# Performance work log

Measured on AMD Instinct MI355X. Metric: run time of the kernel, lower is better.

Reference implementation:

```python
import jax, jax.numpy as jnp
import numpy as np

B, N, D, H = 4, 2048, 512, 8
HD = D // H


def setup_inputs() -> dict:
    key = jax.random.key(0)
    ks = jax.random.split(key, 10)
    x = jax.random.normal(ks[0], (B, N, D), dtype=jnp.float32)
    adj = (jax.random.uniform(ks[1], (N, N)) < 0.1).astype(jnp.float32)
    s = 1.0 / np.sqrt(D)
    Wq = jax.random.normal(ks[2], (D, D), dtype=jnp.float32) * s
    Wk = jax.random.normal(ks[3], (D, D), dtype=jnp.float32) * s
    Wv = jax.random.normal(ks[4], (D, D), dtype=jnp.float32) * s
    Wo = jax.random.normal(ks[5], (D, D), dtype=jnp.float32) * s
    bq = jnp.zeros((D,), jnp.float32)
    bk = jnp.zeros((D,), jnp.float32)
    bv = jnp.zeros((D,), jnp.float32)
    bo = jnp.zeros((D,), jnp.float32)
    return {"x": x, "adj": adj, "Wq": Wq, "bq": bq, "Wk": Wk, "bk": bk,
            "Wv": Wv, "bv": bv, "Wo": Wo, "bo": bo}


def reference(x, adj, Wq, bq, Wk, bk, Wv, bv, Wo, bo):
    b, n, d = x.shape
    q = (x @ Wq + bq).reshape(b, n, H, HD)
    k = (x @ Wk + bk).reshape(b, n, H, HD)
    v = (x @ Wv + bv).reshape(b, n, H, HD)
    scores = jnp.einsum('bqhd,bkhd->bhqk', q, k) / jnp.sqrt(jnp.float32(HD))
    scores = scores + (1.0 - adj)[None, None, :, :] * (-1e9)
    attn = jax.nn.softmax(scores, axis=-1)
    out = jnp.einsum('bhqk,bkhd->bqhd', attn, v).reshape(b, n, d)
    return out @ Wo + bo
```

## Files before the change

### kernel.cpp

```cpp
#include <hip/hip_runtime.h>
#include <math.h>

#define NB    4
#define NSEQ  2048
#define DMODEL 512
#define NH    8
#define HDIM  64
#define STR   72
#define LOG2E 1.44269504088896f

typedef __attribute__((ext_vector_type(8))) short short8;
typedef __attribute__((ext_vector_type(4))) float f32x4;
typedef __attribute__((ext_vector_type(16))) float f32x16;
#define MFMA16 __builtin_amdgcn_mfma_f32_16x16x32_bf16
#define MFMA32 __builtin_amdgcn_mfma_f32_32x32x16_bf16
#define EXP2F __builtin_amdgcn_exp2f

__device__ __forceinline__ unsigned short f2bf(float f) {
    union { float f; unsigned int u; } v; v.f = f;
    unsigned int u = v.u;
    unsigned int r = (u + 0x7FFFu + ((u >> 16) & 1u)) >> 16;
    return (unsigned short)r;
}
__device__ __forceinline__ short8 andmask8(short8 p, unsigned bits) {
    union { short8 s; uint4 u; } x; x.s = p;
    x.u.x &= ((bits &   1u) ? 0xFFFFu : 0u) | ((bits &   2u) ? 0xFFFF0000u : 0u);
    x.u.y &= ((bits &   4u) ? 0xFFFFu : 0u) | ((bits &   8u) ? 0xFFFF0000u : 0u);
    x.u.z &= ((bits &  16u) ? 0xFFFFu : 0u) | ((bits &  32u) ? 0xFFFF0000u : 0u);
    x.u.w &= ((bits &  64u) ? 0xFFFFu : 0u) | ((bits & 128u) ? 0xFFFF0000u : 0u);
    return x.s;
}
__device__ __forceinline__ void async16(void* lds, const void* g) {
    __builtin_amdgcn_global_load_lds(
        (const __attribute__((address_space(1))) unsigned int*)g,
        (__attribute__((address_space(3))) unsigned int*)lds, 16, 0, 0);
}

__global__ __launch_bounds__(256) void mask_kernel(const float* __restrict__ adj,
                                                   unsigned long long* __restrict__ Mb) {
    const int w    = blockIdx.x * 4 + (threadIdx.x >> 6);
    const int lane = threadIdx.x & 63;
    const int q  = w >> 5;
    const int kt = w & 31;
    float a = adj[(size_t)q * NSEQ + kt * 64 + lane];
    unsigned long long m = __ballot(a > 0.5f);
    if (lane == 0) Mb[(size_t)kt * NSEQ + q] = m;
}

__global__ __launch_bounds__(256) void split_x_kernel(const float* __restrict__ x,
                                                      unsigned short* __restrict__ xhi) {
    int gid = blockIdx.x * 256 + threadIdx.x;
    float4 a = ((const float4*)x)[gid];
    ushort4 h4;
    h4.x = f2bf(a.x); h4.y = f2bf(a.y); h4.z = f2bf(a.z); h4.w = f2bf(a.w);
    ((ushort4*)xhi)[gid] = h4;
}

__global__ __launch_bounds__(256) void split_wt_kernel(
    const float* __restrict__ Wq, const float* __restrict__ Wk,
    const float* __restrict__ Wv, const float* __restrict__ Wo,
    unsigned short* __restrict__ Wthi)
{
    __shared__ float tile[32][33];
    const int m = blockIdx.z;
    const float* W = (m == 0) ? Wq : (m == 1) ? Wk : (m == 2) ? Wv : Wo;
    const int k0 = blockIdx.x * 32, n0 = blockIdx.y * 32;
    const int tx = threadIdx.x & 31, ty = threadIdx.x >> 5;
    #pragma unroll
    for (int i = 0; i < 4; ++i)
        tile[ty * 4 + i][tx] = W[(size_t)(k0 + ty * 4 + i) * DMODEL + n0 + tx];
    __syncthreads();
    const size_t base = ((size_t)m * DMODEL) * DMODEL;
    #pragma unroll
    for (int i = 0; i < 4; ++i) {
        float f = tile[tx][ty * 4 + i];
        size_t idx = base + (size_t)(n0 + ty * 4 + i) * DMODEL + k0 + tx;
        Wthi[idx] = f2bf(f);
    }
}

__device__ __forceinline__ void gemm_k_loop(
    const unsigned short* __restrict__ Ah,
    const unsigned short* __restrict__ Bh,
    char* smem, f32x4 acc[4][4])
{
    const int t    = threadIdx.x;
    const int lane = t & 63;
    const int wid  = t >> 6;
    const int quad = lane >> 4, l16 = lane & 15;
    const int wm   = wid >> 1,  wn  = wid & 1;

    unsigned short* As_h = (unsigned short*)(smem);
    unsigned short* Bs_h = (unsigned short*)(smem + 8192);

    const int ci0 = t, ci1 = 256 + t;
    const int r0 = ci0 >> 2, r1 = ci1 >> 2;
    const int c0 = (ci0 & 3) ^ ((r0 >> 1) & 3);
    const int c1 = (ci1 & 3) ^ ((r1 >> 1) & 3);
    const char* gAh = (const char*)Ah;
    const char* gBh = (const char*)Bh;
    const int ca = quad ^ ((l16 >> 1) & 3);

    for (int k0 = 0; k0 < DMODEL; k0 += 32) {
        const int kb = k0 * 2;
        async16(As_h + ci0 * 8, gAh + r0 * 1024 + kb + c0 * 16);
        async16(As_h + ci1 * 8, gAh + r1 * 1024 + kb + c1 * 16);
        async16(Bs_h + ci0 * 8, gBh + r0 * 1024 + kb + c0 * 16);
        async16(Bs_h + ci1 * 8, gBh + r1 * 1024 + kb + c1 * 16);
        __syncthreads();

        short8 ah[4], bh[4];
        #pragma unroll
        for (int i = 0; i < 4; ++i) {
            const int Ra = wm * 64 + i * 16 + l16;
            ah[i] = *(const short8*)(As_h + Ra * 32 + ca * 8);
            const int Rb = wn * 64 + i * 16 + l16;
            bh[i] = *(const short8*)(Bs_h + Rb * 32 + ca * 8);
        }
        #pragma unroll
        for (int mi = 0; mi < 4; ++mi)
            #pragma unroll
            for (int ni = 0; ni < 4; ++ni)
                acc[mi][ni] = MFMA16(ah[mi], bh[ni], acc[mi][ni], 0, 0, 0);
        __syncthreads();
    }
}

__global__ __launch_bounds__(256, 2) void qkv_mfma_kernel(
    const unsigned short* __restrict__ xhi,
    const unsigned short* __restrict__ Wthi,
    const float* __restrict__ bq, const float* __restrict__ bk, const float* __restrict__ bv,
    unsigned short* __restrict__ Qhi,
    unsigned short* __restrict__ Khi,
    unsigned short* __restrict__ Vt)
{
    __shared__ __align__(16) char smem[33280];
    const int t    = threadIdx.x;
    const int lane = t & 63;
    const int wid  = t >> 6;
    const int quad = lane >> 4, l16 = lane & 15;
    const int wm   = wid >> 1,  wn  = wid & 1;

    const int row0 = blockIdx.x * 128;
    const int yb   = blockIdx.y;
    const int mtx  = yb >> 2;
    const int col0 = (yb & 3) * 128;

    f32x4 acc[4][4];
    #pragma unroll
    for (int i = 0; i < 4; ++i)
        #pragma unroll
        for (int j = 0; j < 4; ++j) acc[i][j] = (f32x4){0.f, 0.f, 0.f, 0.f};

    const size_t wslot = (size_t)mtx * DMODEL * DMODEL;
    gemm_k_loop(xhi + (size_t)row0 * DMODEL,
                Wthi + wslot + (size_t)col0 * DMODEL, smem, acc);

    const float* bias = (mtx == 0) ? bq : (mtx == 1) ? bk : bv;
    float bcol[4];
    #pragma unroll
    for (int ni = 0; ni < 4; ++ni) bcol[ni] = bias[col0 + wn * 64 + ni * 16 + l16];
    const int h = (col0 + wn * 64) >> 6;

    if (mtx < 2) {
        const float scale = (mtx == 0) ? (0.125f * LOG2E) : 1.0f;
        unsigned short* hig = (mtx == 0) ? Qhi : Khi;
        #pragma unroll
        for (int mi = 0; mi < 4; ++mi) {
            #pragma unroll
            for (int reg = 0; reg < 4; ++reg) {
                const int r = row0 + wm * 64 + mi * 16 + quad * 4 + reg;
                const int b = r >> 11, n = r & 2047;
                const size_t rowbase = ((size_t)(b * NH + h) * NSEQ + n) * HDIM;
                #pragma unroll
                for (int ni = 0; ni < 4; ++ni)
                    hig[rowbase + ni * 16 + l16] =
                        f2bf((acc[mi][ni][reg] + bcol[ni]) * scale);
            }
        }
    } else {
        unsigned short* vt = (unsigned short*)smem + (size_t)wid * 64 * 65;
        #pragma unroll
        for (int mi = 0; mi < 4; ++mi)
            #pragma unroll
            for (int ni = 0; ni < 4; ++ni)
                #pragma unroll
                for (int reg = 0; reg < 4; ++reg)
                    vt[(mi * 16 + quad * 4 + reg) * 65 + ni * 16 + l16] =
                        f2bf(acc[mi][ni][reg] + bcol[ni]);
        const int b   = row0 >> 11;
        const int n0g = (row0 & 2047) + wm * 64;
        const int bh  = b * NH + h;
        unsigned short* gdst = Vt + ((size_t)bh * HDIM + lane) * NSEQ + n0g;
        #pragma unroll
        for (int nb = 0; nb < 8; ++nb) {
            unsigned short v[8];
            #pragma unroll
            for (int j = 0; j < 8; ++j) v[j] = vt[(nb * 8 + j) * 65 + lane];
            uint4 u;
            u.x = (unsigned)v[0] | ((unsigned)v[1] << 16);
            u.y = (unsigned)v[2] | ((unsigned)v[3] << 16);
            u.z = (unsigned)v[4] | ((unsigned)v[5] << 16);
            u.w = (unsigned)v[6] | ((unsigned)v[7] << 16);
            *(uint4*)(gdst + nb * 8) = u;
        }
    }
}

__global__ __launch_bounds__(256, 2) void out_mfma_kernel(
    const unsigned short* __restrict__ chi,
    const unsigned short* __restrict__ Wthi,
    const float* __restrict__ bo, float* __restrict__ out)
{
    __shared__ __align__(16) char smem[16384];
    const int t    = threadIdx.x;
    const int lane = t & 63;
    const int wid  = t >> 6;
    const int quad = lane >> 4, l16 = lane & 15;
    const int wm   = wid >> 1,  wn  = wid & 1;

    const int row0 = blockIdx.x * 128;
    const int col0 = blockIdx.y * 128;

    f32x4 acc[4][4];
    #pragma unroll
    for (int i = 0; i < 4; ++i)
        #pragma unroll
        for (int j = 0; j < 4; ++j) acc[i][j] = (f32x4){0.f, 0.f, 0.f, 0.f};

    const size_t wslot = (size_t)3 * DMODEL * DMODEL;
    gemm_k_loop(chi + (size_t)row0 * DMODEL,
                Wthi + wslot + (size_t)col0 * DMODEL, smem, acc);

    float bcol[4];
    #pragma unroll
    for (int ni = 0; ni < 4; ++ni) bcol[ni] = bo[col0 + wn * 64 + ni * 16 + l16];
    #pragma unroll
    for (int mi = 0; mi < 4; ++mi)
        #pragma unroll
        for (int reg = 0; reg < 4; ++reg) {
            const int r = row0 + wm * 64 + mi * 16 + quad * 4 + reg;
            float* orow = out + (size_t)r * DMODEL + col0 + wn * 64 + l16;
            #pragma unroll
            for (int ni = 0; ni < 4; ++ni)
                orow[ni * 16] = acc[mi][ni][reg] + bcol[ni];
        }
}

__global__ __launch_bounds__(256) void attn_kernel(
    const unsigned short* __restrict__ Qhi,
    const unsigned short* __restrict__ Khi,
    const unsigned short* __restrict__ Vt,
    const unsigned long long* __restrict__ Mb,
    float* __restrict__ Opart, float* __restrict__ lpart)
{
    __shared__ __align__(16) unsigned short KS[64 * STR];
    __shared__ __align__(16) unsigned short VS[64 * STR];
    __shared__ __align__(16) unsigned short PS[4][32 * STR];

    const int t    = threadIdx.x;
    const int wq   = t >> 6;
    const int lane = t & 63;
    const int l32  = lane & 31;
    const int hw   = lane >> 5;
    const int q0   = blockIdx.x * 128;
    const int h    = blockIdx.y;
    const int z    = blockIdx.z;
    const int b    = z >> 1;
    const int ks   = z & 1;
    const int bh   = b * NH + h;
    const int qa   = q0 + wq * 32;

    short8 qh[4];
    #pragma unroll
    for (int s = 0; s < 4; ++s)
        qh[s] = *(const short8*)(Qhi + ((size_t)bh * NSEQ + qa + l32) * HDIM + s * 16 + hw * 8);
    const unsigned long long* mrow = Mb + (qa + l32);

    short8 onesf;
    #pragma unroll
    for (int i = 0; i < 8; ++i) onesf[i] = (short)0x3F80;

    f32x16 O0, O1, Ol;
    #pragma unroll
    for (int i = 0; i < 16; ++i) { O0[i] = 0.f; O1[i] = 0.f; Ol[i] = 0.f; }

    const unsigned short* gk = Khi + (size_t)bh * NSEQ * HDIM;
    const unsigned short* gv = Vt  + (size_t)bh * HDIM * NSEQ;
    unsigned short* ps = &PS[wq][0];

    const int ci0 = t, ci1 = t + 256;
    const int sr0 = ci0 >> 3, sc0 = (ci0 & 7) * 8;
    const int sr1 = ci1 >> 3, sc1 = (ci1 & 7) * 8;

    for (int kt = ks * 16; kt < ks * 16 + 16; ++kt) {
        const int k0 = kt * 64;
        *(uint4*)&KS[sr0 * STR + sc0] = *(const uint4*)(gk + (size_t)(k0 + sr0) * HDIM + sc0);
        *(uint4*)&KS[sr1 * STR + sc1] = *(const uint4*)(gk + (size_t)(k0 + sr1) * HDIM + sc1);
        *(uint4*)&VS[sr0 * STR + sc0] = *(const uint4*)(gv + (size_t)sr0 * NSEQ + k0 + sc0);
        *(uint4*)&VS[sr1 * STR + sc1] = *(const uint4*)(gv + (size_t)sr1 * NSEQ + k0 + sc1);
        __syncthreads();

        const unsigned long long mw = mrow[(size_t)kt * NSEQ];

        #pragma unroll
        for (int nt = 0; nt < 2; ++nt) {
            f32x16 S;
            #pragma unroll
            for (int i = 0; i < 16; ++i) S[i] = 0.f;
            #pragma unroll
            for (int s = 0; s < 4; ++s) {
                short8 kb = *(const short8*)&KS[(nt * 32 + l32) * STR + s * 16 + hw * 8];
                S = MFMA32(qh[s], kb, S, 0, 0, 0);
            }
            #pragma unroll
            for (int r = 0; r < 16; ++r) {
                float p = EXP2F(S[r]);
                const int row = (r & 3) + 8 * (r >> 2) + 4 * hw;
                ps[row * STR + nt * 32 + l32] =
                    (unsigned short)(__float_as_uint(p) >> 16);
            }
        }

        short8 pf[4];
        #pragma unroll
        for (int s = 0; s < 4; ++s) {
            pf[s] = *(const short8*)&ps[l32 * STR + s * 16 + hw * 8];
            pf[s] = andmask8(pf[s], (unsigned)(mw >> (s * 16 + hw * 8)) & 0xFFu);
        }

        #pragma unroll
        for (int s = 0; s < 4; ++s) {
            short8 v0 = *(const short8*)&VS[(l32) * STR + s * 16 + hw * 8];
            short8 v1 = *(const short8*)&VS[(32 + l32) * STR + s * 16 + hw * 8];
            O0 = MFMA32(pf[s], v0, O0, 0, 0, 0);
            O1 = MFMA32(pf[s], v1, O1, 0, 0, 0);
            Ol = MFMA32(pf[s], onesf, Ol, 0, 0, 0);
        }

        __syncthreads();
    }

    const size_t obase = ((size_t)(ks * NB + b) * NH + h) * NSEQ;
    #pragma unroll
    for (int r = 0; r < 16; ++r) {
        const int qrow = qa + (r & 3) + 8 * (r >> 2) + 4 * hw;
        float* orow = Opart + (obase + qrow) * HDIM;
        orow[l32]      = O0[r];
        orow[32 + l32] = O1[r];
        if (l32 == 0) lpart[obase + qrow] = Ol[r];
    }
}

__global__ __launch_bounds__(256) void merge_kernel(
    const float* __restrict__ Opart, const float* __restrict__ lpart,
    unsigned short* __restrict__ chi)
{
    const int g = blockIdx.x * 256 + threadIdx.x;
    const int qitem = g >> 2;
    const int grp = g & 3;
    const size_t HS = (size_t)NB * NH * NSEQ * HDIM;
    const float* pa = Opart + (size_t)qitem * HDIM + grp * 16;
    const float* pb = pa + HS;
    const float inv = 1.0f / (lpart[qitem] + lpart[qitem + NB * NH * NSEQ]);

    const int n = qitem & 2047, h = (qitem >> 11) & 7, b = qitem >> 14;
    unsigned short* dst = chi + ((size_t)b * NSEQ + n) * DMODEL + h * HDIM + grp * 16;

    unsigned short o[16];
    #pragma unroll
    for (int i = 0; i < 16; i += 4) {
        float4 a4 = *(const float4*)(pa + i);
        float4 b4 = *(const float4*)(pb + i);
        o[i + 0] = f2bf((a4.x + b4.x) * inv);
        o[i + 1] = f2bf((a4.y + b4.y) * inv);
        o[i + 2] = f2bf((a4.z + b4.z) * inv);
        o[i + 3] = f2bf((a4.w + b4.w) * inv);
    }
    uint4 u0, u1;
    u0.x = (unsigned)o[0]  | ((unsigned)o[1]  << 16);
    u0.y = (unsigned)o[2]  | ((unsigned)o[3]  << 16);
    u0.z = (unsigned)o[4]  | ((unsigned)o[5]  << 16);
    u0.w = (unsigned)o[6]  | ((unsigned)o[7]  << 16);
    u1.x = (unsigned)o[8]  | ((unsigned)o[9]  << 16);
    u1.y = (unsigned)o[10] | ((unsigned)o[11] << 16);
    u1.z = (unsigned)o[12] | ((unsigned)o[13] << 16);
    u1.w = (unsigned)o[14] | ((unsigned)o[15] << 16);
    *(uint4*)dst = u0;
    *(uint4*)(dst + 8) = u1;
}

extern "C" void kernel_launch(void* const* d_in, const int* in_sizes, int n_in,
                              void* d_out, int out_size, void* d_ws, size_t ws_size,
                              hipStream_t stream) {
    const float* x   = (const float*)d_in[0];
    const float* adj = (const float*)d_in[1];
    const float* Wq  = (const float*)d_in[2];
    const float* bq  = (const float*)d_in[3];
    const float* Wk  = (const float*)d_in[4];
    const float* bk  = (const float*)d_in[5];
    const float* Wv  = (const float*)d_in[6];
    const float* bv  = (const float*)d_in[7];
    const float* Wo  = (const float*)d_in[8];
    const float* bo  = (const float*)d_in[9];
    float* out = (float*)d_out;

    const size_t elems = (size_t)NB * NSEQ * DMODEL;
    unsigned short* Qhi  = (unsigned short*)d_ws;
    unsigned short* Khi  = Qhi + elems;
    unsigned short* Vt   = Khi + elems;
    unsigned long long* Mbits = (unsigned long long*)(Vt + elems);
    unsigned short* xhi  = (unsigned short*)(Mbits + 32 * NSEQ);
    unsigned short* Wthi = xhi + elems;
    float* Opart = (float*)(Wthi + 4 * (size_t)DMODEL * DMODEL);
    float* lpart = Opart + 2 * (size_t)NB * NH * NSEQ * HDIM;
    unsigned short* chi = xhi;

    mask_kernel   <<<dim3(16384), dim3(256), 0, stream>>>(adj, Mbits);
    split_x_kernel<<<dim3(4096), dim3(256), 0, stream>>>(x, xhi);
    split_wt_kernel<<<dim3(16, 16, 4), dim3(256), 0, stream>>>(Wq, Wk, Wv, Wo, Wthi);
    qkv_mfma_kernel<<<dim3(64, 12), dim3(256), 0, stream>>>(
        xhi, Wthi, bq, bk, bv, Qhi, Khi, Vt);
    attn_kernel<<<dim3(NSEQ / 128, NH, NB * 2), dim3(256), 0, stream>>>(
        Qhi, Khi, Vt, Mbits, Opart, lpart);
    merge_kernel<<<dim3(1024), dim3(256), 0, stream>>>(Opart, lpart, chi);
    out_mfma_kernel<<<dim3(64, 4), dim3(256), 0, stream>>>(
        chi, Wthi, bo, out);
}
```

Measured before the change: 203.2 us.

## Double-buffer K/V tiles, keep P in registers via permlane swap, remap blocks

The attention kernel now double-buffers K and V tiles in LDS, prefetching the next tile into registers while the current tile's MFMAs run, and uses one barrier per iteration. It computes S transposed so that the exponentiated P can be packed to bf16 with v_cvt_pk_bf16_f32 and rearranged with permlane32_swap, which removes the per-wave P staging buffer in LDS. It also remaps the flat block index to group heads and batches, sets MFMA priority hints, and adds an occupancy hint to launch bounds. The risks are higher register pressure from the prefetch registers and the packing switching from truncation to round-to-nearest.

```diff
diff --git a/kernel.cpp b/kernel.cpp
--- a/kernel.cpp
+++ b/kernel.cpp
@@ -12,6 +12,7 @@
 typedef __attribute__((ext_vector_type(8))) short short8;
 typedef __attribute__((ext_vector_type(4))) float f32x4;
 typedef __attribute__((ext_vector_type(16))) float f32x16;
+typedef __attribute__((ext_vector_type(2))) unsigned int uint2v;
 #define MFMA16 __builtin_amdgcn_mfma_f32_16x16x32_bf16
 #define MFMA32 __builtin_amdgcn_mfma_f32_32x32x16_bf16
 #define EXP2F __builtin_amdgcn_exp2f
@@ -34,6 +35,15 @@
     __builtin_amdgcn_global_load_lds(
         (const __attribute__((address_space(1))) unsigned int*)g,
         (__attribute__((address_space(3))) unsigned int*)lds, 16, 0, 0);
+}
+__device__ __forceinline__ unsigned cvtpk(float lo, float hi) {
+    unsigned r;
+    asm("v_cvt_pk_bf16_f32 %0, %1, %2" : "=v"(r) : "v"(lo), "v"(hi));
+    return r;
+}
+__device__ __forceinline__ void pswap(unsigned& a, unsigned& b) {
+    uint2v r = __builtin_amdgcn_permlane32_swap(a, b, false, false);
+    a = r[0]; b = r[1];
 }
 
 __global__ __launch_bounds__(256) void mask_kernel(const float* __restrict__ adj,
@@ -247,28 +257,32 @@
         }
 }
 
-__global__ __launch_bounds__(256) void attn_kernel(
+__global__ __launch_bounds__(256, 4) void attn_kernel(
     const unsigned short* __restrict__ Qhi,
     const unsigned short* __restrict__ Khi,
     const unsigned short* __restrict__ Vt,
     const unsigned long long* __restrict__ Mb,
     float* __restrict__ Opart, float* __restrict__ lpart)
 {
-    __shared__ __align__(16) unsigned short KS[64 * STR];
-    __shared__ __align__(16) unsigned short VS[64 * STR];
-    __shared__ __align__(16) unsigned short PS[4][32 * STR];
+    __shared__ __align__(16) unsigned short KS[2][64 * STR];
+    __shared__ __align__(16) unsigned short VS[2][64 * STR];
 
     const int t    = threadIdx.x;
     const int wq   = t >> 6;
     const int lane = t & 63;
     const int l32  = lane & 31;
     const int hw   = lane >> 5;
-    const int q0   = blockIdx.x * 128;
-    const int h    = blockIdx.y;
-    const int z    = blockIdx.z;
+
+    const int flat = blockIdx.x + 16 * (blockIdx.y + 8 * blockIdx.z);
+    const int loc  = flat >> 3;
+    const int yz   = (flat & 7) * 8 + (loc & 7);
+    const int qt   = loc >> 3;
+    const int h    = yz & 7;
+    const int z    = yz >> 3;
     const int b    = z >> 1;
     const int ks   = z & 1;
     const int bh   = b * NH + h;
+    const int q0   = qt * 128;
     const int qa   = q0 + wq * 32;
 
     short8 qh[4];
@@ -287,57 +301,91 @@
 
     const unsigned short* gk = Khi + (size_t)bh * NSEQ * HDIM;
     const unsigned short* gv = Vt  + (size_t)bh * HDIM * NSEQ;
-    unsigned short* ps = &PS[wq][0];
 
     const int ci0 = t, ci1 = t + 256;
     const int sr0 = ci0 >> 3, sc0 = (ci0 & 7) * 8;
     const int sr1 = ci1 >> 3, sc1 = (ci1 & 7) * 8;
 
-    for (int kt = ks * 16; kt < ks * 16 + 16; ++kt) {
-        const int k0 = kt * 64;
-        *(uint4*)&KS[sr0 * STR + sc0] = *(const uint4*)(gk + (size_t)(k0 + sr0) * HDIM + sc0);
-        *(uint4*)&KS[sr1 * STR + sc1] = *(const uint4*)(gk + (size_t)(k0 + sr1) * HDIM + sc1);
-        *(uint4*)&VS[sr0 * STR + sc0] = *(const uint4*)(gv + (size_t)sr0 * NSEQ + k0 + sc0);
-        *(uint4*)&VS[sr1 * STR + sc1] = *(const uint4*)(gv + (size_t)sr1 * NSEQ + k0 + sc1);
-        __syncthreads();
-
+    const int ktBeg = ks * 16, ktEnd = ktBeg + 16;
+
+    {
+        const int k0 = ktBeg * 64;
+        uint4 ka = *(const uint4*)(gk + (size_t)(k0 + sr0) * HDIM + sc0);
+        uint4 kc = *(const uint4*)(gk + (size_t)(k0 + sr1) * HDIM + sc1);
+        uint4 va = *(const uint4*)(gv + (size_t)sr0 * NSEQ + k0 + sc0);
+        uint4 vc = *(const uint4*)(gv + (size_t)sr1 * NSEQ + k0 + sc1);
+        *(uint4*)&KS[0][sr0 * STR + sc0] = ka;
+        *(uint4*)&KS[0][sr1 * STR + sc1] = kc;
+        *(uint4*)&VS[0][sr0 * STR + sc0] = va;
+        *(uint4*)&VS[0][sr1 * STR + sc1] = vc;
+    }
+    __syncthreads();
+
+    for (int kt = ktBeg; kt < ktEnd; ++kt) {
+        const int cur = (kt - ktBeg) & 1;
+        const unsigned short* ksrc = &KS[cur][0];
+        const unsigned short* vsrc = &VS[cur][0];
         const unsigned long long mw = mrow[(size_t)kt * NSEQ];
 
+        short8 pf[4];
         #pragma unroll
         for (int nt = 0; nt < 2; ++nt) {
             f32x16 S;
             #pragma unroll
             for (int i = 0; i < 16; ++i) S[i] = 0.f;
+            __builtin_amdgcn_s_setprio(1);
             #pragma unroll
             for (int s = 0; s < 4; ++s) {
-                short8 kb = *(const short8*)&KS[(nt * 32 + l32) * STR + s * 16 + hw * 8];
-                S = MFMA32(qh[s], kb, S, 0, 0, 0);
+                short8 kb = *(const short8*)&ksrc[(nt * 32 + l32) * STR + s * 16 + hw * 8];
+                S = MFMA32(kb, qh[s], S, 0, 0, 0);
             }
-            #pragma unroll
-            for (int r = 0; r < 16; ++r) {
-                float p = EXP2F(S[r]);
-                const int row = (r & 3) + 8 * (r >> 2) + 4 * hw;
-                ps[row * STR + nt * 32 + l32] =
-                    (unsigned short)(__float_as_uint(p) >> 16);
-            }
-        }
-
-        short8 pf[4];
+            __builtin_amdgcn_s_setprio(0);
+            float p[16];
+            #pragma unroll
+            for (int r = 0; r < 16; ++r) p[r] = EXP2F(S[r]);
+            unsigned w[8];
+            #pragma unroll
+            for (int i = 0; i < 8; ++i) w[i] = cvtpk(p[2 * i], p[2 * i + 1]);
+            pswap(w[0], w[2]); pswap(w[1], w[3]);
+            pswap(w[4], w[6]); pswap(w[5], w[7]);
+            union { short8 s8; unsigned u[4]; } A, B2;
+            A.u[0] = w[0]; A.u[1] = w[1]; A.u[2] = w[2]; A.u[3] = w[3];
+            B2.u[0] = w[4]; B2.u[1] = w[5]; B2.u[2] = w[6]; B2.u[3] = w[7];
+            pf[2 * nt]     = A.s8;
+            pf[2 * nt + 1] = B2.s8;
+        }
+
+        uint4 nk0, nk1, nv0, nv1;
+        const bool more = (kt + 1 < ktEnd);
+        if (more) {
+            const int k0n = (kt + 1) * 64;
+            nk0 = *(const uint4*)(gk + (size_t)(k0n + sr0) * HDIM + sc0);
+            nk1 = *(const uint4*)(gk + (size_t)(k0n + sr1) * HDIM + sc1);
+            nv0 = *(const uint4*)(gv + (size_t)sr0 * NSEQ + k0n + sc0);
+            nv1 = *(const uint4*)(gv + (size_t)sr1 * NSEQ + k0n + sc1);
+        }
+
+        #pragma unroll
+        for (int s = 0; s < 4; ++s)
+            pf[s] = andmask8(pf[s], (unsigned)(mw >> (s * 16 + hw * 8)) & 0xFFu);
+
+        __builtin_amdgcn_s_setprio(1);
         #pragma unroll
         for (int s = 0; s < 4; ++s) {
-            pf[s] = *(const short8*)&ps[l32 * STR + s * 16 + hw * 8];
-            pf[s] = andmask8(pf[s], (unsigned)(mw >> (s * 16 + hw * 8)) & 0xFFu);
-        }
-
-        #pragma unroll
-        for (int s = 0; s < 4; ++s) {
-            short8 v0 = *(const short8*)&VS[(l32) * STR + s * 16 + hw * 8];
-            short8 v1 = *(const short8*)&VS[(32 + l32) * STR + s * 16 + hw * 8];
+            short8 v0 = *(const short8*)&vsrc[(l32) * STR + s * 16 + hw * 8];
+            short8 v1 = *(const short8*)&vsrc[(32 + l32) * STR + s * 16 + hw * 8];
             O0 = MFMA32(pf[s], v0, O0, 0, 0, 0);
             O1 = MFMA32(pf[s], v1, O1, 0, 0, 0);
             Ol = MFMA32(pf[s], onesf, Ol, 0, 0, 0);
         }
-
+        __builtin_amdgcn_s_setprio(0);
+
+        if (more) {
+            *(uint4*)&KS[cur ^ 1][sr0 * STR + sc0] = nk0;
+            *(uint4*)&KS[cur ^ 1][sr1 * STR + sc1] = nk1;
+            *(uint4*)&VS[cur ^ 1][sr0 * STR + sc0] = nv0;
+            *(uint4*)&VS[cur ^ 1][sr1 * STR + sc1] = nv1;
+        }
         __syncthreads();
     }
 
```

Result: faster. 197.7 us (-2.7%).
